# Performance work log

Measured on AMD Instinct MI355X. Metric: run time of the kernel, lower is better.

Reference implementation:

```python
import jax, jax.numpy as jnp
import numpy as np

NUM_CIRC = 5        # circles per vehicle (init kwarg)
BUFFER_DIST = 0.0   # extra separation buffer (init kwarg)


def setup_inputs() -> dict:
    key = jax.random.key(0)
    k1, k2, k3 = jax.random.split(key, 3)
    NA, T = 128, 100  # 8 scenes x 16 agents, 100 timesteps
    traj = jax.random.normal(k1, (NA, T, 4), dtype=jnp.float32)
    # spread positions over ~+-100m so collisions are sparse but present
    traj = traj.at[:, :, :2].multiply(50.0)
    # realistic vehicle attributes: length ~3-5.5m, width ~1.5-2.2m
    length = jax.random.uniform(k2, (NA,), minval=3.0, maxval=5.5, dtype=jnp.float32)
    width = jax.random.uniform(k3, (NA,), minval=1.5, maxval=2.2, dtype=jnp.float32)
    veh_att = jnp.stack([length, width], axis=1)
    ptr = jnp.arange(9) * 16  # 8 scenes of 16 agents each
    return {"traj": traj, "veh_att": veh_att, "ptr": ptr}


def _forward(traj, veh_att, ptr):
    NA, T, _ = traj.shape
    C = NUM_CIRC
    veh_rad = veh_att[:, 1] * 0.5
    half_len = veh_att[:, 0] * 0.5
    cent_min = -half_len + veh_rad
    cent_max = half_len - veh_rad
    # per-vehicle circle centers along the length axis (local frame): NA x C
    frac = jnp.linspace(0.0, 1.0, C, dtype=traj.dtype)
    cent_x = cent_min[:, None] + (cent_max - cent_min)[:, None] * frac[None, :]
    # transform2frame(traj, centroids, inverse=True): rotate local (cx, 0) by the
    # (normalized) heading and translate by position -> world = pos + cx * h_unit
    pos = traj[:, :, :2]                                   # NA,T,2
    h = traj[:, :, 2:4]
    h = h / jnp.linalg.norm(h, axis=-1, keepdims=True)     # unit heading
    world_cent = pos[:, :, None, :] + cent_x[:, None, :, None] * h[:, :, None, :]  # NA,T,C,2
    world_cent = jnp.transpose(world_cent, (1, 0, 2, 3))   # T,NA,C,2
    # pairwise circle distances: T,NA,NA,C,C (matches torch.cdist over circle dims)
    diff = world_cent[:, :, None, :, None, :] - world_cent[:, None, :, None, :, :]
    sq = jnp.sum(diff * diff, axis=-1)
    pos_sq = sq > 0
    dists = jnp.where(pos_sq, jnp.sqrt(jnp.where(pos_sq, sq, 1.0)), 0.0)
    min_pair_dists = jnp.min(dists.reshape(T, NA, NA, C * C), axis=-1)  # T,NA,NA
    penalty_dists = veh_rad[:, None] + veh_rad[None, :] + BUFFER_DIST   # NA,NA
    # valid pairs: same scene (via ptr) and off-diagonal
    scene_id = jnp.searchsorted(ptr[1:], jnp.arange(NA), side="right")
    valid_mask = (scene_id[:, None] == scene_id[None, :]) & ~jnp.eye(NA, dtype=bool)
    colliding = (min_pair_dists <= penalty_dists[None]) & valid_mask[None]
    penalties = jnp.where(colliding, 1.0 - min_pair_dists / penalty_dists[None],
                          jnp.zeros((), dtype=traj.dtype))
    graph_sizes = ptr[1:] - ptr[:-1]
    num_pairs = jnp.sum(graph_sizes * graph_sizes - graph_sizes)
    # NOTE: torch gathers penalties[valid_mask] (dynamic shape); we return the
    # dense T,NA,NA tensor which is zero exactly at invalid entries, so any
    # reduction (sum/mean over valid pairs) matches.
    return penalties, num_pairs


def reference(traj, veh_att, ptr):
    return _forward(traj, veh_att, ptr)
```

## Files before the change

kernel.cpp:

```cpp
#include <hip/hip_runtime.h>

#define NAG 128
#define TT  100
#define NC  5

__global__ __launch_bounds__(256) void vehcoll_kernel(
    const float* __restrict__ traj,
    const float* __restrict__ veh_att,
    const int*   __restrict__ ptr,
    float* __restrict__ out,
    int n_ptr)
{
    __shared__ float s_wcx[NAG][NC];
    __shared__ float s_wcy[NAG][NC];
    __shared__ float s_rad[NAG];
    __shared__ int   s_scene[NAG];

    const int t   = blockIdx.x >> 6;
    const int pb  = blockIdx.x & 63;
    const int tid = threadIdx.x;

    if (tid < NAG) {
        const int a = tid;
        float4 tr = *(const float4*)(traj + ((size_t)a * TT + t) * 4);
        float len = veh_att[a * 2 + 0];
        float wid = veh_att[a * 2 + 1];
        float rad  = 0.5f * wid;
        float cmin = -0.5f * len + rad;
        float step = 0.25f * (len - wid);
        float inv  = 1.0f / sqrtf(tr.z * tr.z + tr.w * tr.w);
        float hx = tr.z * inv, hy = tr.w * inv;
        #pragma unroll
        for (int c = 0; c < NC; ++c) {
            float cx = cmin + step * (float)c;
            s_wcx[a][c] = tr.x + cx * hx;
            s_wcy[a][c] = tr.y + cx * hy;
        }
        s_rad[a] = rad;
        int sc = 0;
        for (int k = 1; k < n_ptr; ++k) sc += (ptr[k] <= a) ? 1 : 0;
        s_scene[a] = sc;
    }
    __syncthreads();

    const int p = pb * 256 + tid;
    const int i = p >> 7;
    const int j = p & 127;

    float pen = 0.0f;
    if (i != j && s_scene[i] == s_scene[j]) {
        float ax[NC], ay[NC], bx[NC], by[NC];
        #pragma unroll
        for (int c = 0; c < NC; ++c) {
            ax[c] = s_wcx[i][c];  ay[c] = s_wcy[i][c];
            bx[c] = s_wcx[j][c];  by[c] = s_wcy[j][c];
        }
        float minsq = 3.4e38f;
        #pragma unroll
        for (int ci = 0; ci < NC; ++ci) {
            #pragma unroll
            for (int cj = 0; cj < NC; ++cj) {
                float dx = ax[ci] - bx[cj];
                float dy = ay[ci] - by[cj];
                minsq = fminf(minsq, dx * dx + dy * dy);
            }
        }
        float d  = sqrtf(minsq);
        float pd = s_rad[i] + s_rad[j];
        if (d <= pd) pen = 1.0f - d / pd;
    }
    out[(size_t)t * NAG * NAG + p] = pen;

    if (blockIdx.x == 0 && tid == 0) {
        int np = 0;
        for (int k = 0; k + 1 < n_ptr; ++k) {
            int g = ptr[k + 1] - ptr[k];
            np += g * g - g;
        }
        out[(size_t)TT * NAG * NAG] = (float)np;
    }
}

extern "C" void kernel_launch(void* const* d_in, const int* in_sizes, int n_in,
                              void* d_out, int out_size, void* d_ws, size_t ws_size,
                              hipStream_t stream) {
    const float* traj    = (const float*)d_in[0];
    const float* veh_att = (const float*)d_in[1];
    const int*   ptr     = (const int*)d_in[2];
    float*       out     = (float*)d_out;
    const int n_ptr = in_sizes[2];

    dim3 grid(TT * 64);
    dim3 block(256);
    hipLaunchKernelGGL(vehcoll_kernel, grid, block, 0, stream,
                       traj, veh_att, ptr, out, n_ptr);
}
```

Baseline: 67.30 us.

## Compute four pairs per thread with float4 stores and transposed circle layout

Each thread now computes four consecutive j-pairs for one i, reusing the i circle centers held in registers. The grid shrinks fourfold, so the per-block shared-memory setup (trajectory loads, scene search) is repeated across fewer blocks. Outputs are written as one float4 per thread, and circle centers are stored circle-major so neighbouring agents sit contiguously in shared memory. This amortises setup cost and widens stores, at the cost of more registers and fewer blocks to spread across the GPU.

```diff
diff --git a/kernel.cpp b/kernel.cpp
--- a/kernel.cpp
+++ b/kernel.cpp
@@ -3,6 +3,9 @@
 #define NAG 128
 #define TT  100
 #define NC  5
+#define PB_PER_T 16
+#define PAIRS_PER_BLOCK 1024
+#define PPT 4
 
 __global__ __launch_bounds__(256) void vehcoll_kernel(
     const float* __restrict__ traj,
@@ -11,13 +14,13 @@
     float* __restrict__ out,
     int n_ptr)
 {
-    __shared__ float s_wcx[NAG][NC];
-    __shared__ float s_wcy[NAG][NC];
+    __shared__ float s_cx[NC][NAG];
+    __shared__ float s_cy[NC][NAG];
     __shared__ float s_rad[NAG];
     __shared__ int   s_scene[NAG];
 
-    const int t   = blockIdx.x >> 6;
-    const int pb  = blockIdx.x & 63;
+    const int t   = blockIdx.x >> 4;
+    const int pb  = blockIdx.x & 15;
     const int tid = threadIdx.x;
 
     if (tid < NAG) {
@@ -26,15 +29,15 @@
         float len = veh_att[a * 2 + 0];
         float wid = veh_att[a * 2 + 1];
         float rad  = 0.5f * wid;
-        float cmin = -0.5f * len + rad;
+        float cmin = rad - 0.5f * len;
         float step = 0.25f * (len - wid);
         float inv  = 1.0f / sqrtf(tr.z * tr.z + tr.w * tr.w);
         float hx = tr.z * inv, hy = tr.w * inv;
         #pragma unroll
         for (int c = 0; c < NC; ++c) {
             float cx = cmin + step * (float)c;
-            s_wcx[a][c] = tr.x + cx * hx;
-            s_wcy[a][c] = tr.y + cx * hy;
+            s_cx[c][a] = tr.x + cx * hx;
+            s_cy[c][a] = tr.y + cx * hy;
         }
         s_rad[a] = rad;
         int sc = 0;
@@ -43,33 +46,39 @@
     }
     __syncthreads();
 
-    const int p = pb * 256 + tid;
-    const int i = p >> 7;
-    const int j = p & 127;
+    const int p0 = pb * PAIRS_PER_BLOCK + tid * PPT;
+    const int i  = p0 >> 7;
+    const int j0 = p0 & 127;
 
-    float pen = 0.0f;
-    if (i != j && s_scene[i] == s_scene[j]) {
-        float ax[NC], ay[NC], bx[NC], by[NC];
+    float pen[PPT] = {0.f, 0.f, 0.f, 0.f};
+    const int sci = s_scene[i];
+    if (sci >= s_scene[j0] && sci <= s_scene[j0 + PPT - 1]) {
+        float ix[NC], iy[NC];
         #pragma unroll
-        for (int c = 0; c < NC; ++c) {
-            ax[c] = s_wcx[i][c];  ay[c] = s_wcy[i][c];
-            bx[c] = s_wcx[j][c];  by[c] = s_wcy[j][c];
+        for (int c = 0; c < NC; ++c) { ix[c] = s_cx[c][i]; iy[c] = s_cy[c][i]; }
+        const float ri = s_rad[i];
+        #pragma unroll
+        for (int q = 0; q < PPT; ++q) {
+            const int j = j0 + q;
+            float minsq = 3.4e38f;
+            #pragma unroll
+            for (int ci = 0; ci < NC; ++ci) {
+                const float jxc = 0.0f; (void)jxc;
+                #pragma unroll
+                for (int cj = 0; cj < NC; ++cj) {
+                    float dx = ix[ci] - s_cx[cj][j];
+                    float dy = iy[ci] - s_cy[cj][j];
+                    minsq = fminf(minsq, dx * dx + dy * dy);
+                }
+            }
+            float d  = sqrtf(minsq);
+            float pd = ri + s_rad[j];
+            bool valid = (i != j) && (sci == s_scene[j]);
+            pen[q] = (valid && d <= pd) ? 1.0f - d / pd : 0.0f;
         }
-        float minsq = 3.4e38f;
-        #pragma unroll
-        for (int ci = 0; ci < NC; ++ci) {
-            #pragma unroll
-            for (int cj = 0; cj < NC; ++cj) {
-                float dx = ax[ci] - bx[cj];
-                float dy = ay[ci] - by[cj];
-                minsq = fminf(minsq, dx * dx + dy * dy);
-            }
-        }
-        float d  = sqrtf(minsq);
-        float pd = s_rad[i] + s_rad[j];
-        if (d <= pd) pen = 1.0f - d / pd;
     }
-    out[(size_t)t * NAG * NAG + p] = pen;
+    *(float4*)(out + (size_t)t * NAG * NAG + p0) =
+        make_float4(pen[0], pen[1], pen[2], pen[3]);
 
     if (blockIdx.x == 0 && tid == 0) {
         int np = 0;
@@ -90,7 +99,7 @@
     float*       out     = (float*)d_out;
     const int n_ptr = in_sizes[2];
 
-    dim3 grid(TT * 64);
+    dim3 grid(TT * PB_PER_T);
     dim3 block(256);
     hipLaunchKernelGGL(vehcoll_kernel, grid, block, 0, stream,
                        traj, veh_att, ptr, out, n_ptr);
```

New measurement: 66.80 us. No clear change (-0.7%).
